# Kernel tuning notes

Measured on AMD Instinct MI355X. Metric: run time of the kernel, lower is better.

Reference implementation:

```python
import jax, jax.numpy as jnp
import numpy as np

N_NODES = 50000
N_EDGES = 1600000
H_DIM = 128
OUT_DIM = 128
N_RELS = 16


def setup_inputs() -> dict:
    key = jax.random.key(0)
    k1, k2, k3, k4, k5, k6 = jax.random.split(key, 6)
    node_ids = jnp.arange(N_NODES, dtype=jnp.int64) if jax.config.jax_enable_x64 else jnp.arange(N_NODES, dtype=jnp.int32)
    src = jax.random.randint(k1, (N_EDGES,), 0, N_NODES, dtype=jnp.int32)
    dst = jax.random.randint(k2, (N_EDGES,), 0, N_NODES, dtype=jnp.int32)
    rel = jax.random.randint(k3, (N_EDGES,), 0, N_RELS, dtype=jnp.int32)
    norm = jax.random.uniform(k4, (N_EDGES, 1), dtype=jnp.float32)
    emb_table = jax.random.normal(k5, (N_NODES, H_DIM), dtype=jnp.float32)
    W = jax.random.normal(k6, (N_RELS, H_DIM, OUT_DIM), dtype=jnp.float32) * (1.0 / np.sqrt(H_DIM))
    return {"node_ids": node_ids, "src": src, "dst": dst, "rel": rel,
            "norm": norm, "emb_table": emb_table, "W": W}


def reference(node_ids, src, dst, rel, norm, emb_table, W):
    # Input layer: embedding lookup on node ids.  [N, h_dim]
    h = emb_table[node_ids]
    n_nodes = emb_table.shape[0]
    # RelGraphConv (full per-relation weight, no basis, no self-loop,
    # activation=None for the single/last layer, dropout inactive at eval):
    # Transform all node features by every relation weight up front
    # (R small, avoids [E, d, o] per-edge weight gather).  [R, N, out]
    h_rel = jnp.einsum('nd,rdo->rno', h, W)
    # Gather per-edge transformed source features, apply edge norm.  [E, out]
    msg = h_rel[rel, src] * norm
    # Scatter-sum messages to destination nodes.  [N, out]
    out = jax.ops.segment_sum(msg, dst, num_segments=n_nodes)
    return out
```

## Files before the change

### kernel.cpp

```cpp
#include <hip/hip_runtime.h>
#include <hip/hip_bf16.h>

#define NN 50000
#define NE 1600000
#define HD 128
#define NR 16
#define NCB 1563
#define S2B 512
#define EPB (NE / S2B)
#define SLOT 2048
#define TOTSLOT 3200000
#define PREPH_BLKS 6250
#define PREPW_BLKS 1024
#define GEMM_BLKS 1564

typedef __bf16 bf16x8 __attribute__((ext_vector_type(8)));
typedef unsigned short u16x8 __attribute__((ext_vector_type(8)));
typedef float f32x4 __attribute__((ext_vector_type(4)));

__device__ __forceinline__ unsigned short f2bf(float f) {
    union { float f; unsigned int u; } v; v.f = f;
    unsigned int u = v.u;
    u += 0x7FFFu + ((u >> 16) & 1u);
    return (unsigned short)(u >> 16);
}
__device__ __forceinline__ float bflo(unsigned int u) {
    union { unsigned int u; float f; } v; v.u = u << 16; return v.f;
}
__device__ __forceinline__ float bfhi(unsigned int u) {
    union { unsigned int u; float f; } v; v.u = u & 0xFFFF0000u; return v.f;
}

__global__ __launch_bounds__(256) void prep_all(const int* __restrict__ node_ids,
                                                const float* __restrict__ emb,
                                                unsigned short* __restrict__ h_bf,
                                                const float* __restrict__ W,
                                                unsigned short* __restrict__ Wt,
                                                const int* __restrict__ dst,
                                                int* __restrict__ cntM) {
    const int b = blockIdx.x;
    const int t = threadIdx.x;
    if (b < PREPH_BLKS) {
        int gid = b * 256 + t;
        int row = gid >> 5;
        int c = (gid & 31) << 2;
        int nid = node_ids[row];
        if (nid < 0) nid = 0; if (nid >= NN) nid = NN - 1;
        float4 v = *(const float4*)(emb + (size_t)nid * HD + c);
        ushort4 o;
        o.x = f2bf(v.x); o.y = f2bf(v.y); o.z = f2bf(v.z); o.w = f2bf(v.w);
        *(ushort4*)(h_bf + (size_t)row * HD + c) = o;
    } else if (b < PREPH_BLKS + PREPW_BLKS) {
        int gid = (b - PREPH_BLKS) * 256 + t;
        int r = gid >> 14;
        int idx = gid & 16383;
        int k = idx >> 7;
        int o = idx & 127;
        Wt[(size_t)r * 16384 + (size_t)o * 128 + k] = f2bf(W[gid]);
    } else {
        __shared__ int h[NCB];
        const int sb = b - PREPH_BLKS - PREPW_BLKS;
        for (int i = t; i < NCB; i += 256) h[i] = 0;
        __syncthreads();
        const int base = sb * EPB;
        for (int i = t; i < EPB; i += 256)
            atomicAdd(&h[((unsigned)dst[base + i]) >> 5], 1);
        __syncthreads();
        for (int i = t; i < NCB; i += 256) cntM[sb * NCB + i] = h[i];
    }
}

__global__ __launch_bounds__(256) void scanBins(int* __restrict__ cntM,
                                                int* __restrict__ binN) {
    __shared__ int s[256];
    const int t = threadIdx.x;
    const int bin = blockIdx.x;
    int v0 = cntM[(2 * t) * NCB + bin];
    int v1 = cntM[(2 * t + 1) * NCB + bin];
    s[t] = v0 + v1;
    __syncthreads();
    for (int off = 1; off < 256; off <<= 1) {
        int x = (t >= off) ? s[t - off] : 0;
        __syncthreads();
        s[t] += x;
        __syncthreads();
    }
    int total = s[255];
    int e0 = s[t] - v0 - v1;
    int e1 = e0 + v0;
    int cap = (bin == NCB - 1) ? (TOTSLOT - (NCB - 1) * SLOT) : SLOT;
    cntM[(2 * t) * NCB + bin]     = bin * SLOT + (e0 < cap ? e0 : cap);
    cntM[(2 * t + 1) * NCB + bin] = bin * SLOT + (e1 < cap ? e1 : cap);
    if (t == 255) binN[bin] = (total < cap) ? total : cap;
}

__global__ __launch_bounds__(256) void s2gemm(const int* __restrict__ src,
                                              const int* __restrict__ dst,
                                              const int* __restrict__ rel,
                                              const float* __restrict__ norm,
                                              const int* __restrict__ cntM,
                                              uint2* __restrict__ recs,
                                              const unsigned short* __restrict__ h_bf,
                                              const unsigned short* __restrict__ Wt,
                                              unsigned short* __restrict__ h_rel) {
    __shared__ unsigned short sA[128][136];
    __shared__ unsigned short sB[128][136];
    __shared__ int cur[NCB];
    const int b = blockIdx.x;
    const int t = threadIdx.x;

    if (b < 2048 && (b & 3) == 3) {
        const int sb = b >> 2;
        for (int i = t; i < NCB; i += 256) cur[i] = cntM[sb * NCB + i];
        __syncthreads();
        const int base = sb * EPB;
        for (int i = t; i < EPB; i += 256) {
            int e = base + i;
            int d = dst[e];
            int bin = ((unsigned)d) >> 5;
            int p = atomicAdd(&cur[bin], 1);
            int binEnd = (bin == NCB - 1) ? TOTSLOT : (bin + 1) * SLOT;
            if (p < binEnd) {
                unsigned x = (unsigned)src[e] | ((unsigned)rel[e] << 16)
                           | ((unsigned)(d & 31) << 20);
                recs[p] = make_uint2(x, __float_as_uint(norm[e]));
            }
        }
        return;
    }

    const int g = (b < 2048) ? (b - ((b + 1) >> 2)) : (b - S2B);
    const int tile = g % 391;
    const int rg = g / 391;
    const int base = tile * 128;

    #pragma unroll
    for (int j = 0; j < 8; ++j) {
        int idx = t + j * 256;
        int row = idx >> 4;
        int c8 = (idx & 15) << 3;
        int gg = base + row;
        if (gg >= NN) gg = 0;
        uint4 v = *(const uint4*)(h_bf + (size_t)gg * 128 + c8);
        *(uint4*)&sA[row][c8] = v;
    }

    const int lane = t & 63;
    const int w = t >> 6;
    const int wr = w >> 1, wc = w & 1;
    const int l15 = lane & 15, lhi = lane >> 4;

    for (int rr = 0; rr < 4; ++rr) {
        const int r = rg * 4 + rr;
        if (rr > 0) __syncthreads();
        const unsigned short* wp = Wt + ((size_t)r << 14);
        #pragma unroll
        for (int j = 0; j < 8; ++j) {
            int idx = t + j * 256;
            int row = idx >> 4;
            int c8 = (idx & 15) << 3;
            uint4 v = *(const uint4*)(wp + (size_t)row * 128 + c8);
            *(uint4*)&sB[row][c8] = v;
        }
        __syncthreads();

        f32x4 acc[4][4];
        #pragma unroll
        for (int i = 0; i < 4; ++i)
            #pragma unroll
            for (int j = 0; j < 4; ++j)
                acc[i][j] = (f32x4){0.f, 0.f, 0.f, 0.f};

        #pragma unroll
        for (int kt = 0; kt < 4; ++kt) {
            const int ko = kt * 32 + lhi * 8;
            bf16x8 aF[4], bF[4];
            #pragma unroll
            for (int ms = 0; ms < 4; ++ms) {
                u16x8 raw = *(const u16x8*)&sA[wr * 64 + ms * 16 + l15][ko];
                aF[ms] = __builtin_bit_cast(bf16x8, raw);
            }
            #pragma unroll
            for (int nt = 0; nt < 4; ++nt) {
                u16x8 raw = *(const u16x8*)&sB[wc * 64 + nt * 16 + l15][ko];
                bF[nt] = __builtin_bit_cast(bf16x8, raw);
            }
            #pragma unroll
            for (int ms = 0; ms < 4; ++ms)
                #pragma unroll
                for (int nt = 0; nt < 4; ++nt)
                    acc[ms][nt] = __builtin_amdgcn_mfma_f32_16x16x32_bf16(
                        aF[ms], bF[nt], acc[ms][nt], 0, 0, 0);
        }

        #pragma unroll
        for (int ms = 0; ms < 4; ++ms) {
            #pragma unroll
            for (int reg = 0; reg < 4; ++reg) {
                int m = base + wr * 64 + ms * 16 + lhi * 4 + reg;
                if (m < NN) {
                    size_t rowp = ((size_t)r * NN + m) * 128;
                    #pragma unroll
                    for (int nt = 0; nt < 4; ++nt) {
                        int o = wc * 64 + nt * 16 + l15;
                        h_rel[rowp + o] = f2bf(acc[ms][nt][reg]);
                    }
                }
            }
        }
    }
}

__global__ __launch_bounds__(256) void seg_fused(const int* __restrict__ binN,
                                                 const uint2* __restrict__ recs,
                                                 const unsigned int* __restrict__ hb,
                                                 float* __restrict__ out) {
    __shared__ uint2 rec[SLOT];
    __shared__ unsigned char sub8[SLOT];
    __shared__ unsigned short idx16[SLOT];
    __shared__ int h[32], sbx[33], cur[32];
    const int t = threadIdx.x;
    const int bin = blockIdx.x;
    const int n = binN[bin];
    const uint2* rg = recs + (size_t)bin * SLOT;

    if (t < 32) h[t] = 0;
    __syncthreads();
    for (int i = t; i < n; i += 256) {
        uint2 r = rg[i];
        int sub = (r.x >> 20) & 31;
        rec[i] = make_uint2(((r.x >> 16) & 15) * (unsigned)NN + (r.x & 0xFFFFu),
                            r.y);
        sub8[i] = (unsigned char)sub;
        atomicAdd(&h[sub], 1);
    }
    __syncthreads();
    if (t == 0) {
        int run = 0;
        #pragma unroll
        for (int s = 0; s < 32; ++s) { sbx[s] = run; run += h[s]; }
        sbx[32] = run;
    }
    __syncthreads();
    if (t < 32) cur[t] = sbx[t];
    __syncthreads();
    for (int i = t; i < n; i += 256) {
        int p = atomicAdd(&cur[sub8[i]], 1);
        idx16[p] = (unsigned short)i;
    }
    __syncthreads();

    const int lane = t & 63;
    const int w = t >> 6;
    #pragma unroll
    for (int k = 0; k < 8; ++k) {
        int j = w * 8 + k;
        int d = bin * 32 + j;
        if (d >= NN) continue;
        int beg = sbx[j], end = sbx[j + 1];
        float a0 = 0.f, a1 = 0.f;
        int i = beg;
        for (; i + 7 < end; i += 8) {
            int i0 = idx16[i],     i1 = idx16[i + 1];
            int i2 = idx16[i + 2], i3 = idx16[i + 3];
            int i4 = idx16[i + 4], i5 = idx16[i + 5];
            int i6 = idx16[i + 6], i7 = idx16[i + 7];
            uint2 r0 = rec[i0], r1 = rec[i1], r2 = rec[i2], r3 = rec[i3];
            uint2 r4 = rec[i4], r5 = rec[i5], r6 = rec[i6], r7 = rec[i7];
            unsigned u0 = hb[r0.x * 64u + lane];
            unsigned u1 = hb[r1.x * 64u + lane];
            unsigned u2 = hb[r2.x * 64u + lane];
            unsigned u3 = hb[r3.x * 64u + lane];
            unsigned u4 = hb[r4.x * 64u + lane];
            unsigned u5 = hb[r5.x * 64u + lane];
            unsigned u6 = hb[r6.x * 64u + lane];
            unsigned u7 = hb[r7.x * 64u + lane];
            float n0 = __uint_as_float(r0.y), n1 = __uint_as_float(r1.y);
            float n2 = __uint_as_float(r2.y), n3 = __uint_as_float(r3.y);
            float n4 = __uint_as_float(r4.y), n5 = __uint_as_float(r5.y);
            float n6 = __uint_as_float(r6.y), n7 = __uint_as_float(r7.y);
            a0 += bflo(u0) * n0 + bflo(u1) * n1 + bflo(u2) * n2 + bflo(u3) * n3;
            a1 += bfhi(u0) * n0 + bfhi(u1) * n1 + bfhi(u2) * n2 + bfhi(u3) * n3;
            a0 += bflo(u4) * n4 + bflo(u5) * n5 + bflo(u6) * n6 + bflo(u7) * n7;
            a1 += bfhi(u4) * n4 + bfhi(u5) * n5 + bfhi(u6) * n6 + bfhi(u7) * n7;
        }
        for (; i < end; ++i) {
            uint2 rc = rec[idx16[i]];
            unsigned u = hb[rc.x * 64u + lane];
            float nm = __uint_as_float(rc.y);
            a0 += bflo(u) * nm;
            a1 += bfhi(u) * nm;
        }
        *(float2*)(out + (size_t)d * 128 + lane * 2) = make_float2(a0, a1);
    }
}


extern "C" void kernel_launch(void* const* d_in, const int* in_sizes, int n_in,
                              void* d_out, int out_size, void* d_ws, size_t ws_size,
                              hipStream_t stream) {
    const int* node_ids = (const int*)d_in[0];
    const int* src      = (const int*)d_in[1];
    const int* dst      = (const int*)d_in[2];
    const int* rel      = (const int*)d_in[3];
    const float* norm   = (const float*)d_in[4];
    const float* emb    = (const float*)d_in[5];
    const float* W      = (const float*)d_in[6];
    float* out = (float*)d_out;

    char* ws = (char*)d_ws;
    unsigned short* h_rel = (unsigned short*)(ws);
    unsigned short* h_bf  = (unsigned short*)(ws + 204800000);
    unsigned short* Wt    = (unsigned short*)(ws + 217600000);
    int* cntM             = (int*)(ws + 218124288);
    int* binN             = (int*)(ws + 221325312);

    uint2* recs = (uint2*)d_out;

    prep_all<<<PREPH_BLKS + PREPW_BLKS + S2B, 256, 0, stream>>>(
        node_ids, emb, h_bf, W, Wt, dst, cntM);
    scanBins<<<NCB, 256, 0, stream>>>(cntM, binN);
    s2gemm<<<S2B + GEMM_BLKS, 256, 0, stream>>>(src, dst, rel, norm, cntM, recs,
                                                h_bf, Wt, h_rel);
    seg_fused<<<NCB, 256, 0, stream>>>(binN, recs,
                                       (const unsigned int*)h_rel, out);
}
```

Baseline: 312.1 us.

## Split scatter from GEMM and stage GEMM output through LDS for coalesced stores

Separates the combined edge-scatter/GEMM kernel into two kernels: a dedicated scatter kernel and a GEMM kernel on a 2D grid. The GEMM epilogue now writes bf16 results into shared memory and then issues 16-byte coalesced row stores to h_rel, replacing the scattered 2-byte global stores. This targets store inefficiency on the large h_rel write, but adds two barriers per relation and loses the overlap that came from co-scheduling the scatter and GEMM blocks in one launch.

```diff
diff --git a/kernel.cpp b/kernel.cpp
--- a/kernel.cpp
+++ b/kernel.cpp
@@ -12,7 +12,6 @@
 #define TOTSLOT 3200000
 #define PREPH_BLKS 6250
 #define PREPW_BLKS 1024
-#define GEMM_BLKS 1564
 
 typedef __bf16 bf16x8 __attribute__((ext_vector_type(8)));
 typedef unsigned short u16x8 __attribute__((ext_vector_type(8)));
@@ -94,54 +93,48 @@
     if (t == 255) binN[bin] = (total < cap) ? total : cap;
 }
 
-__global__ __launch_bounds__(256) void s2gemm(const int* __restrict__ src,
-                                              const int* __restrict__ dst,
-                                              const int* __restrict__ rel,
-                                              const float* __restrict__ norm,
-                                              const int* __restrict__ cntM,
-                                              uint2* __restrict__ recs,
-                                              const unsigned short* __restrict__ h_bf,
-                                              const unsigned short* __restrict__ Wt,
-                                              unsigned short* __restrict__ h_rel) {
+__global__ __launch_bounds__(256) void s2_scatter(const int* __restrict__ src,
+                                                  const int* __restrict__ dst,
+                                                  const int* __restrict__ rel,
+                                                  const float* __restrict__ norm,
+                                                  const int* __restrict__ cntM,
+                                                  uint2* __restrict__ recs) {
+    __shared__ int cur[NCB];
+    const int t = threadIdx.x, sb = blockIdx.x;
+    for (int i = t; i < NCB; i += 256) cur[i] = cntM[sb * NCB + i];
+    __syncthreads();
+    const int base = sb * EPB;
+    for (int i = t; i < EPB; i += 256) {
+        int e = base + i;
+        int d = dst[e];
+        int bin = ((unsigned)d) >> 5;
+        int p = atomicAdd(&cur[bin], 1);
+        int binEnd = (bin == NCB - 1) ? TOTSLOT : (bin + 1) * SLOT;
+        if (p < binEnd) {
+            unsigned x = (unsigned)src[e] | ((unsigned)rel[e] << 16)
+                       | ((unsigned)(d & 31) << 20);
+            recs[p] = make_uint2(x, __float_as_uint(norm[e]));
+        }
+    }
+}
+
+__global__ __launch_bounds__(256) void gemm_hrel(const unsigned short* __restrict__ h_bf,
+                                                 const unsigned short* __restrict__ Wt,
+                                                 unsigned short* __restrict__ h_rel) {
     __shared__ unsigned short sA[128][136];
     __shared__ unsigned short sB[128][136];
-    __shared__ int cur[NCB];
-    const int b = blockIdx.x;
     const int t = threadIdx.x;
-
-    if (b < 2048 && (b & 3) == 3) {
-        const int sb = b >> 2;
-        for (int i = t; i < NCB; i += 256) cur[i] = cntM[sb * NCB + i];
-        __syncthreads();
-        const int base = sb * EPB;
-        for (int i = t; i < EPB; i += 256) {
-            int e = base + i;
-            int d = dst[e];
-            int bin = ((unsigned)d) >> 5;
-            int p = atomicAdd(&cur[bin], 1);
-            int binEnd = (bin == NCB - 1) ? TOTSLOT : (bin + 1) * SLOT;
-            if (p < binEnd) {
-                unsigned x = (unsigned)src[e] | ((unsigned)rel[e] << 16)
-                           | ((unsigned)(d & 31) << 20);
-                recs[p] = make_uint2(x, __float_as_uint(norm[e]));
-            }
-        }
-        return;
-    }
-
-    const int g = (b < 2048) ? (b - ((b + 1) >> 2)) : (b - S2B);
-    const int tile = g % 391;
-    const int rg = g / 391;
-    const int base = tile * 128;
+    const int base = blockIdx.x * 128;
+    const int rg = blockIdx.y;
 
     #pragma unroll
     for (int j = 0; j < 8; ++j) {
         int idx = t + j * 256;
         int row = idx >> 4;
         int c8 = (idx & 15) << 3;
-        int gg = base + row;
-        if (gg >= NN) gg = 0;
-        uint4 v = *(const uint4*)(h_bf + (size_t)gg * 128 + c8);
+        int g = base + row;
+        if (g >= NN) g = 0;
+        uint4 v = *(const uint4*)(h_bf + (size_t)g * 128 + c8);
         *(uint4*)&sA[row][c8] = v;
     }
 
@@ -193,19 +186,25 @@
                         aF[ms], bF[nt], acc[ms][nt], 0, 0, 0);
         }
 
-        #pragma unroll
-        for (int ms = 0; ms < 4; ++ms) {
-            #pragma unroll
-            for (int reg = 0; reg < 4; ++reg) {
-                int m = base + wr * 64 + ms * 16 + lhi * 4 + reg;
-                if (m < NN) {
-                    size_t rowp = ((size_t)r * NN + m) * 128;
-                    #pragma unroll
-                    for (int nt = 0; nt < 4; ++nt) {
-                        int o = wc * 64 + nt * 16 + l15;
-                        h_rel[rowp + o] = f2bf(acc[ms][nt][reg]);
-                    }
-                }
+        __syncthreads();
+        #pragma unroll
+        for (int ms = 0; ms < 4; ++ms)
+            #pragma unroll
+            for (int nt = 0; nt < 4; ++nt)
+                #pragma unroll
+                for (int reg = 0; reg < 4; ++reg)
+                    sB[wr * 64 + ms * 16 + lhi * 4 + reg]
+                      [wc * 64 + nt * 16 + l15] = f2bf(acc[ms][nt][reg]);
+        __syncthreads();
+        size_t rbase = ((size_t)r * NN + base) * 128;
+        #pragma unroll
+        for (int j = 0; j < 8; ++j) {
+            int idx = t + j * 256;
+            int row = idx >> 4;
+            int c8 = (idx & 15) << 3;
+            if (base + row < NN) {
+                uint4 v = *(const uint4*)&sB[row][c8];
+                *(uint4*)(h_rel + rbase + (size_t)row * 128 + c8) = v;
             }
         }
     }
@@ -320,8 +319,8 @@
     prep_all<<<PREPH_BLKS + PREPW_BLKS + S2B, 256, 0, stream>>>(
         node_ids, emb, h_bf, W, Wt, dst, cntM);
     scanBins<<<NCB, 256, 0, stream>>>(cntM, binN);
-    s2gemm<<<S2B + GEMM_BLKS, 256, 0, stream>>>(src, dst, rel, norm, cntM, recs,
-                                                h_bf, Wt, h_rel);
+    s2_scatter<<<S2B, 256, 0, stream>>>(src, dst, rel, norm, cntM, recs);
+    gemm_hrel<<<dim3(391, 4), 256, 0, stream>>>(h_bf, Wt, h_rel);
     seg_fused<<<NCB, 256, 0, stream>>>(binN, recs,
                                        (const unsigned int*)h_rel, out);
 }
```

Measured after the change: 301.0 us. 1.04x faster.
